# Optimization experiments

Hardware: AMD Instinct MI355X
Metric: run time of the kernel (lower is better)

The kernel has to match this reference:

```python
import jax, jax.numpy as jnp
import numpy as np

N, E = 20000, 640000
IN_CH, OUT_CH = 128, 64
HEADS = (4, 4)
NEG_SLOPE = 0.2


def _gat_layer(x, src, dst, edge_attr, edge_atten, W, a_src, a_dst, W_e, a_e, b, H, C, n_nodes):
    # x: [N, F_in] -> per-head features [N, H, C]
    xh = (x @ W).reshape(-1, H, C)
    alpha_src = jnp.sum(xh * a_src, axis=-1)          # [N, H]
    alpha_dst = jnp.sum(xh * a_dst, axis=-1)          # [N, H]
    eemb = (edge_attr @ W_e).reshape(-1, H, C)        # [E, H, C]
    alpha_e = jnp.sum(eemb * a_e, axis=-1)            # [E, H]
    alpha = alpha_src[src] + alpha_dst[dst] + alpha_e # [E, H]
    alpha = jax.nn.leaky_relu(alpha, NEG_SLOPE)
    # softmax over variable-degree neighborhoods (segments keyed by dst)
    amax = jax.ops.segment_max(alpha, dst, num_segments=n_nodes)
    alpha = jnp.exp(alpha - amax[dst])
    denom = jax.ops.segment_sum(alpha, dst, num_segments=n_nodes)
    alpha = alpha / (denom[dst] + 1e-16)
    msg = xh[src] * alpha[:, :, None]                 # [E, H, C]
    msg = msg * edge_atten[:, :, None]                # edge_atten: [E, 1] -> broadcast over H, C
    out = jax.ops.segment_sum(msg, dst, num_segments=n_nodes)
    out = out.reshape(n_nodes, H * C) + b
    return out, alpha


def setup_inputs() -> dict:
    key = jax.random.key(0)
    ks = jax.random.split(key, 16)
    H1, H2 = HEADS
    d1_in, d1_out = IN_CH, H1 * OUT_CH
    d2_in, d2_out = H1 * OUT_CH, H2 * OUT_CH
    s = lambda fi: 1.0 / np.sqrt(fi)
    inp = {
        "x": jax.random.normal(ks[0], (N, IN_CH), jnp.float32),
        "edge_index": jax.random.randint(ks[1], (2, E), 0, N, jnp.int64 if jax.config.jax_enable_x64 else jnp.int32),
        "batch": jnp.zeros((N,), jnp.int32),
        "edge_attr": jax.random.normal(ks[2], (E, 1), jnp.float32),
        "edge_atten": jax.random.uniform(ks[3], (E, 1), jnp.float32),
        # layer 1 params
        "W1": jax.random.normal(ks[4], (d1_in, d1_out), jnp.float32) * s(d1_in),
        "a_src1": jax.random.normal(ks[5], (H1, OUT_CH), jnp.float32) * s(OUT_CH),
        "a_dst1": jax.random.normal(ks[6], (H1, OUT_CH), jnp.float32) * s(OUT_CH),
        "W_e1": jax.random.normal(ks[7], (1, d1_out), jnp.float32),
        "a_e1": jax.random.normal(ks[8], (H1, OUT_CH), jnp.float32) * s(OUT_CH),
        "b1": jnp.zeros((d1_out,), jnp.float32),
        # layer 2 params
        "W2": jax.random.normal(ks[9], (d2_in, d2_out), jnp.float32) * s(d2_in),
        "a_src2": jax.random.normal(ks[10], (H2, OUT_CH), jnp.float32) * s(OUT_CH),
        "a_dst2": jax.random.normal(ks[11], (H2, OUT_CH), jnp.float32) * s(OUT_CH),
        "W_e2": jax.random.normal(ks[12], (1, d2_out), jnp.float32),
        "a_e2": jax.random.normal(ks[13], (H2, OUT_CH), jnp.float32) * s(OUT_CH),
        "b2": jnp.zeros((d2_out,), jnp.float32),
    }
    return inp


def reference(x, edge_index, batch, edge_attr, edge_atten,
              W1, a_src1, a_dst1, W_e1, a_e1, b1,
              W2, a_src2, a_dst2, W_e2, a_e2, b2):
    src, dst = edge_index[0], edge_index[1]
    h, w1 = _gat_layer(x, src, dst, edge_attr, edge_atten,
                       W1, a_src1, a_dst1, W_e1, a_e1, b1, HEADS[0], OUT_CH, N)
    h, w2 = _gat_layer(h, src, dst, edge_attr, edge_atten,
                       W2, a_src2, a_dst2, W_e2, a_e2, b2, HEADS[1], OUT_CH, N)
    return h, w1, w2
```

## Files before the change

kernel.cpp:

```cpp
#include <hip/hip_runtime.h>
#include <math.h>

#define NEG_SLOPE 0.2f
#define CAP 128
#define ST  136
#define NNODES 20000
#define NB 128

typedef short s16x8 __attribute__((ext_vector_type(8)));
typedef unsigned short us8 __attribute__((ext_vector_type(8)));
typedef float f32x4 __attribute__((ext_vector_type(4)));

__device__ __forceinline__ unsigned short f2bf(float f) {
    unsigned int u = __float_as_uint(f);
    return (unsigned short)((u + 0x7FFFu + ((u >> 16) & 1u)) >> 16);
}
__device__ __forceinline__ float bf2f(unsigned short s) {
    return __uint_as_float(((unsigned int)s) << 16);
}

__global__ __launch_bounds__(512) void hist_prep(const int* __restrict__ dst,
                                                 int* __restrict__ ghist,
                                                 int E, int chunk, int N, int histB,
                                                 const float* __restrict__ x,
                                                 const float* __restrict__ W1,
                                                 const float* __restrict__ W2,
                                                 const float* __restrict__ W_e1,
                                                 const float* __restrict__ a_e1,
                                                 const float* __restrict__ W_e2,
                                                 const float* __restrict__ a_e2,
                                                 unsigned short* __restrict__ xb16,
                                                 unsigned short* __restrict__ Wt1,
                                                 unsigned short* __restrict__ Wt2,
                                                 float* __restrict__ ce) {
    __shared__ int h[NNODES / 2];
    if ((int)blockIdx.x < histB) {
        const int b = blockIdx.x;
        const int NH = N >> 1;
        for (int i = threadIdx.x; i < NH; i += 512) h[i] = 0;
        __syncthreads();
        const int e0 = b * chunk;
        const int e1 = min(e0 + chunk, E);
        for (int e = e0 + (int)threadIdx.x; e < e1; e += 512) {
            int d = dst[e];
            atomicAdd(&h[d >> 1], 1 << ((d & 1) << 4));
        }
        __syncthreads();
        int2* out = (int2*)(ghist + (size_t)b * N);
        for (int i = threadIdx.x; i < NH; i += 512) {
            int v = h[i];
            out[i] = make_int2(v & 0xFFFF, ((unsigned)v) >> 16);
        }
    } else {
        const int p = (int)blockIdx.x - histB;
        const int gsz = 256 * 512;
        const int gid = p * 512 + (int)threadIdx.x;
        for (int i = gid; i < 128 * 256; i += gsz) {
            int k = i >> 8, n = i & 255;
            Wt1[n * 128 + k] = f2bf(W1[i]);
        }
        for (int i = gid; i < 256 * 256; i += gsz) {
            int k = i >> 8, n = i & 255;
            Wt2[n * 256 + k] = f2bf(W2[i]);
        }
        for (int i = gid; i < N * 32; i += gsz) {
            float4 f = ((const float4*)x)[i];
            ushort4 u = make_ushort4(f2bf(f.x), f2bf(f.y), f2bf(f.z), f2bf(f.w));
            ((ushort4*)xb16)[i] = u;
        }
        if (p < 2 && threadIdx.x < 256) {
            const float* We = p == 0 ? W_e1 : W_e2;
            const float* ae = p == 0 ? a_e1 : a_e2;
            int hh = threadIdx.x >> 6, c = threadIdx.x & 63;
            float pr = We[hh * 64 + c] * ae[hh * 64 + c];
#pragma unroll
            for (int off = 32; off > 0; off >>= 1) pr += __shfl_down(pr, off);
            if (c == 0) ce[p * 4 + hh] = pr;
        }
    }
}

__global__ __launch_bounds__(1024) void scan_kernel(const int* __restrict__ deg,
                                                    int* __restrict__ off, int N) {
    __shared__ int wsum[16];
    __shared__ int woff[16];
    __shared__ int s_carry, s_bt;
    if (threadIdx.x == 0) s_carry = 0;
    __syncthreads();
    const int lane = threadIdx.x & 63, wid = threadIdx.x >> 6;
    for (int base = 0; base < N; base += 4096) {
        int i0 = base + (int)threadIdx.x * 4;
        int v0 = (i0 + 0 < N) ? deg[i0 + 0] : 0;
        int v1 = (i0 + 1 < N) ? deg[i0 + 1] : 0;
        int v2 = (i0 + 2 < N) ? deg[i0 + 2] : 0;
        int v3 = (i0 + 3 < N) ? deg[i0 + 3] : 0;
        int tsum = v0 + v1 + v2 + v3;
        int incl = tsum;
#pragma unroll
        for (int ofs = 1; ofs < 64; ofs <<= 1) {
            int t = __shfl_up(incl, ofs);
            if (lane >= ofs) incl += t;
        }
        if (lane == 63) wsum[wid] = incl;
        __syncthreads();
        if (wid == 0) {
            int ws = (lane < 16) ? wsum[lane] : 0;
            int wincl = ws;
#pragma unroll
            for (int ofs = 1; ofs < 16; ofs <<= 1) {
                int t = __shfl_up(wincl, ofs);
                if (lane >= ofs) wincl += t;
            }
            if (lane < 16) woff[lane] = wincl - ws;
            if (lane == 15) s_bt = wincl;
        }
        __syncthreads();
        int e0 = s_carry + woff[wid] + incl - tsum;
        int e1 = e0 + v0, e2 = e1 + v1, e3 = e2 + v2;
        if (i0 + 0 < N) off[i0 + 0] = e0;
        if (i0 + 1 < N) off[i0 + 1] = e1;
        if (i0 + 2 < N) off[i0 + 2] = e2;
        if (i0 + 3 < N) off[i0 + 3] = e3;
        __syncthreads();
        if (threadIdx.x == 0) s_carry += s_bt;
        __syncthreads();
    }
    if (threadIdx.x == 0) off[N] = s_carry;
}

__device__ __forceinline__ void gemm_core(const unsigned short* __restrict__ A16,
                                          const unsigned short* __restrict__ Bt16,
                                          unsigned short* __restrict__ C16,
                                          const float* __restrict__ a_src,
                                          const float* __restrict__ a_dst,
                                          float* __restrict__ asrc,
                                          float* __restrict__ adst,
                                          int M, int K, int bx, int by,
                                          unsigned short (*As)[40],
                                          unsigned short (*Bs)[40]) {
    const int tid = threadIdx.x;
    const int w = tid >> 6, l = tid & 63;
    const int quad = l >> 4, m16 = l & 15;
    const int row0 = by * 128, col0 = bx * 64;

    f32x4 acc[2][4] = {};

    const int a_r = tid >> 1;
    const int a_k = (tid & 1) * 16;
    const int b_n = tid >> 2;
    const int b_k = (tid & 3) * 8;

    for (int k0 = 0; k0 < K; k0 += 32) {
        int gr = row0 + a_r; if (gr > M - 1) gr = M - 1;
        const unsigned short* ap = A16 + (size_t)gr * K + k0 + a_k;
        *(us8*)&As[a_r][a_k]     = *(const us8*)ap;
        *(us8*)&As[a_r][a_k + 8] = *(const us8*)(ap + 8);
        *(us8*)&Bs[b_n][b_k] = *(const us8*)(Bt16 + (size_t)(col0 + b_n) * K + k0 + b_k);
        __syncthreads();

        s16x8 af[2], bfr[4];
#pragma unroll
        for (int mt = 0; mt < 2; ++mt)
            af[mt] = *(const s16x8*)&As[w * 32 + mt * 16 + m16][quad * 8];
#pragma unroll
        for (int nt = 0; nt < 4; ++nt)
            bfr[nt] = *(const s16x8*)&Bs[nt * 16 + m16][quad * 8];
#pragma unroll
        for (int mt = 0; mt < 2; ++mt)
#pragma unroll
            for (int nt = 0; nt < 4; ++nt)
                acc[mt][nt] = __builtin_amdgcn_mfma_f32_16x16x32_bf16(af[mt], bfr[nt], acc[mt][nt], 0, 0, 0);
        __syncthreads();
    }

    const int h = bx;
    float was[4], wad[4];
#pragma unroll
    for (int nt = 0; nt < 4; ++nt) {
        int c = nt * 16 + m16;
        was[nt] = a_src[h * 64 + c];
        wad[nt] = a_dst[h * 64 + c];
    }

#pragma unroll
    for (int mt = 0; mt < 2; ++mt)
#pragma unroll
        for (int i = 0; i < 4; ++i) {
            int row = row0 + w * 32 + mt * 16 + quad * 4 + i;
            float ps = 0.f, pd = 0.f;
#pragma unroll
            for (int nt = 0; nt < 4; ++nt) {
                float v = acc[mt][nt][i];
                ps += v * was[nt];
                pd += v * wad[nt];
            }
#pragma unroll
            for (int ofs = 1; ofs < 16; ofs <<= 1) {
                ps += __shfl_xor(ps, ofs);
                pd += __shfl_xor(pd, ofs);
            }
            if (m16 == 0 && row < M) {
                asrc[(size_t)row * 4 + h] = ps;
                adst[(size_t)row * 4 + h] = pd;
            }
        }

#pragma unroll
    for (int mt = 0; mt < 2; ++mt)
#pragma unroll
        for (int nt = 0; nt < 4; ++nt) {
            int col = col0 + nt * 16 + m16;
#pragma unroll
            for (int i = 0; i < 4; ++i) {
                int row = row0 + w * 32 + mt * 16 + quad * 4 + i;
                if (row < M) C16[(size_t)row * 256 + col] = f2bf(acc[mt][nt][i]);
            }
        }
}

__global__ __launch_bounds__(256) void gemm1_scan(const unsigned short* __restrict__ A16,
                                                  const unsigned short* __restrict__ Bt16,
                                                  unsigned short* __restrict__ C16,
                                                  const float* __restrict__ a_src,
                                                  const float* __restrict__ a_dst,
                                                  float* __restrict__ asrc,
                                                  float* __restrict__ adst,
                                                  int M, int K, int gemmB,
                                                  int* __restrict__ ghist,
                                                  int* __restrict__ deg,
                                                  int N, int histB) {
    __shared__ unsigned short As[128][40];
    __shared__ unsigned short Bs[64][40];
    if ((int)blockIdx.x < gemmB) {
        gemm_core(A16, Bt16, C16, a_src, a_dst, asrc, adst, M, K,
                  blockIdx.x & 3, blockIdx.x >> 2, As, Bs);
    } else {
        int bin = ((int)blockIdx.x - gemmB) * 256 + (int)threadIdx.x;
        if (bin < N) {
            int run = 0;
            for (int b = 0; b < histB; b += 8) {
                int v[8];
#pragma unroll
                for (int j = 0; j < 8; ++j) v[j] = ghist[(b + j) * N + bin];
#pragma unroll
                for (int j = 0; j < 8; ++j) { ghist[(b + j) * N + bin] = run; run += v[j]; }
            }
            deg[bin] = run;
        }
    }
}

__global__ __launch_bounds__(1024) void fill2(const int* __restrict__ src,
                                              const int* __restrict__ dst,
                                              const float* __restrict__ edge_attr,
                                              const float* __restrict__ edge_atten,
                                              const int* __restrict__ off,
                                              const int* __restrict__ ghist,
                                              int4* __restrict__ rec,
                                              int E, int chunk, int N) {
    __shared__ int base[NNODES];
    const int b = blockIdx.x;
    const int* part = ghist + (size_t)b * N;
    for (int i = threadIdx.x; i < N; i += 1024) base[i] = off[i] + part[i];
    __syncthreads();
    const int e0 = b * chunk;
    const int e1 = min(e0 + chunk, E);
    for (int e = e0 + (int)threadIdx.x; e < e1; e += 1024) {
        int d = dst[e];
        int pos = atomicAdd(&base[d], 1);
        rec[pos] = make_int4(src[e], e, __float_as_int(edge_attr[e]),
                             __float_as_int(edge_atten[e]));
    }
}

__global__ __launch_bounds__(256) void node_fused(const int4* __restrict__ rec,
                                                  const int* __restrict__ off,
                                                  const float* __restrict__ asrc,
                                                  const float* __restrict__ adst,
                                                  const float* __restrict__ ce,
                                                  const unsigned short* __restrict__ xh16,
                                                  const float* __restrict__ bias,
                                                  float* __restrict__ w,
                                                  int write_w,
                                                  float* __restrict__ mxrc,
                                                  float* __restrict__ houtf,
                                                  unsigned short* __restrict__ hout16,
                                                  int N) {
    __shared__ float s_al[4][4][ST];
    __shared__ int s_src[4][CAP];
    const int wid = threadIdx.x >> 6;
    const int n = blockIdx.x * 4 + wid;
    if (n >= N) return;
    const int lane = threadIdx.x & 63;
    float* al = &s_al[wid][0][0];
    int* sv = s_src[wid];
    const int o0 = off[n], o1 = off[n + 1];
    const int deg = o1 - o0;

    const float4 c4 = *(const float4*)ce;
    const float4 ad4 = *(const float4*)(adst + (size_t)n * 4);

    if (deg <= 64) {
        int4 r; float4 a;
        a.x = a.y = a.z = a.w = -3.4e38f;
        if (lane < deg) {
            r = rec[o0 + lane];
            float ea = __int_as_float(r.z);
            const float4 as4 = *(const float4*)(asrc + (size_t)r.x * 4);
            a.x = as4.x + ad4.x + ea * c4.x;
            a.y = as4.y + ad4.y + ea * c4.y;
            a.z = as4.z + ad4.z + ea * c4.z;
            a.w = as4.w + ad4.w + ea * c4.w;
            a.x = a.x > 0.f ? a.x : NEG_SLOPE * a.x;
            a.y = a.y > 0.f ? a.y : NEG_SLOPE * a.y;
            a.z = a.z > 0.f ? a.z : NEG_SLOPE * a.z;
            a.w = a.w > 0.f ? a.w : NEG_SLOPE * a.w;
        }
        float4 mx = a;
#pragma unroll
        for (int ofs = 1; ofs < 64; ofs <<= 1) {
            mx.x = fmaxf(mx.x, __shfl_xor(mx.x, ofs));
            mx.y = fmaxf(mx.y, __shfl_xor(mx.y, ofs));
            mx.z = fmaxf(mx.z, __shfl_xor(mx.z, ofs));
            mx.w = fmaxf(mx.w, __shfl_xor(mx.w, ofs));
        }
        float4 ex = make_float4(0.f, 0.f, 0.f, 0.f);
        if (lane < deg) {
            ex.x = __expf(a.x - mx.x);
            ex.y = __expf(a.y - mx.y);
            ex.z = __expf(a.z - mx.z);
            ex.w = __expf(a.w - mx.w);
        }
        float4 sm = ex;
#pragma unroll
        for (int ofs = 1; ofs < 64; ofs <<= 1) {
            sm.x += __shfl_xor(sm.x, ofs);
            sm.y += __shfl_xor(sm.y, ofs);
            sm.z += __shfl_xor(sm.z, ofs);
            sm.w += __shfl_xor(sm.w, ofs);
        }
        float4 rc;
        rc.x = 1.f / (sm.x + 1e-16f);
        rc.y = 1.f / (sm.y + 1e-16f);
        rc.z = 1.f / (sm.z + 1e-16f);
        rc.w = 1.f / (sm.w + 1e-16f);
        if (mxrc && lane == 0) {
            *(float4*)(mxrc + (size_t)n * 8) = mx;
            *(float4*)(mxrc + (size_t)n * 8 + 4) = rc;
        }
        if (lane < deg) {
            float4 aln;
            aln.x = ex.x * rc.x;
            aln.y = ex.y * rc.y;
            aln.z = ex.z * rc.z;
            aln.w = ex.w * rc.w;
            if (write_w) *(float4*)(w + (size_t)r.y * 4) = aln;
            float att = __int_as_float(r.w);
            sv[lane] = r.x;
            al[0 * ST + lane] = aln.x * att;
            al[1 * ST + lane] = aln.y * att;
            al[2 * ST + lane] = aln.z * att;
            al[3 * ST + lane] = aln.w * att;
        }
    } else {
        float4 mx = make_float4(-3.4e38f, -3.4e38f, -3.4e38f, -3.4e38f);
        for (int idx = lane; idx < deg; idx += 64) {
            int4 r = rec[o0 + idx];
            float ea = __int_as_float(r.z);
            const float4 as4 = *(const float4*)(asrc + (size_t)r.x * 4);
            float4 a;
            a.x = as4.x + ad4.x + ea * c4.x;
            a.y = as4.y + ad4.y + ea * c4.y;
            a.z = as4.z + ad4.z + ea * c4.z;
            a.w = as4.w + ad4.w + ea * c4.w;
            a.x = a.x > 0.f ? a.x : NEG_SLOPE * a.x;
            a.y = a.y > 0.f ? a.y : NEG_SLOPE * a.y;
            a.z = a.z > 0.f ? a.z : NEG_SLOPE * a.z;
            a.w = a.w > 0.f ? a.w : NEG_SLOPE * a.w;
            if (idx < CAP) {
                sv[idx] = r.x;
                al[0 * ST + idx] = a.x;
                al[1 * ST + idx] = a.y;
                al[2 * ST + idx] = a.z;
                al[3 * ST + idx] = a.w;
            } else {
                *(float4*)(w + (size_t)r.y * 4) = a;
            }
            mx.x = fmaxf(mx.x, a.x);
            mx.y = fmaxf(mx.y, a.y);
            mx.z = fmaxf(mx.z, a.z);
            mx.w = fmaxf(mx.w, a.w);
        }
#pragma unroll
        for (int ofs = 1; ofs < 64; ofs <<= 1) {
            mx.x = fmaxf(mx.x, __shfl_xor(mx.x, ofs));
            mx.y = fmaxf(mx.y, __shfl_xor(mx.y, ofs));
            mx.z = fmaxf(mx.z, __shfl_xor(mx.z, ofs));
            mx.w = fmaxf(mx.w, __shfl_xor(mx.w, ofs));
        }
        float4 sm = make_float4(0.f, 0.f, 0.f, 0.f);
        for (int idx = lane; idx < deg; idx += 64) {
            float4 a;
            int espill = -1;
            if (idx < CAP) {
                a.x = al[0 * ST + idx];
                a.y = al[1 * ST + idx];
                a.z = al[2 * ST + idx];
                a.w = al[3 * ST + idx];
            } else {
                espill = rec[o0 + idx].y;
                a = *(const float4*)(w + (size_t)espill * 4);
            }
            a.x = __expf(a.x - mx.x);
            a.y = __expf(a.y - mx.y);
            a.z = __expf(a.z - mx.z);
            a.w = __expf(a.w - mx.w);
            if (idx < CAP) {
                al[0 * ST + idx] = a.x;
                al[1 * ST + idx] = a.y;
                al[2 * ST + idx] = a.z;
                al[3 * ST + idx] = a.w;
            } else {
                *(float4*)(w + (size_t)espill * 4) = a;
            }
            sm.x += a.x; sm.y += a.y; sm.z += a.z; sm.w += a.w;
        }
#pragma unroll
        for (int ofs = 1; ofs < 64; ofs <<= 1) {
            sm.x += __shfl_xor(sm.x, ofs);
            sm.y += __shfl_xor(sm.y, ofs);
            sm.z += __shfl_xor(sm.z, ofs);
            sm.w += __shfl_xor(sm.w, ofs);
        }
        float4 rc;
        rc.x = 1.f / (sm.x + 1e-16f);
        rc.y = 1.f / (sm.y + 1e-16f);
        rc.z = 1.f / (sm.z + 1e-16f);
        rc.w = 1.f / (sm.w + 1e-16f);
        if (mxrc && lane == 0) {
            *(float4*)(mxrc + (size_t)n * 8) = mx;
            *(float4*)(mxrc + (size_t)n * 8 + 4) = rc;
        }
        for (int idx = lane; idx < deg; idx += 64) {
            int4 r = rec[o0 + idx];
            float4 ex;
            if (idx < CAP) {
                ex.x = al[0 * ST + idx];
                ex.y = al[1 * ST + idx];
                ex.z = al[2 * ST + idx];
                ex.w = al[3 * ST + idx];
            } else {
                ex = *(const float4*)(w + (size_t)r.y * 4);
            }
            float4 aln;
            aln.x = ex.x * rc.x;
            aln.y = ex.y * rc.y;
            aln.z = ex.z * rc.z;
            aln.w = ex.w * rc.w;
            *(float4*)(w + (size_t)r.y * 4) = aln;
            if (idx < CAP) {
                float att = __int_as_float(r.w);
                al[0 * ST + idx] = aln.x * att;
                al[1 * ST + idx] = aln.y * att;
                al[2 * ST + idx] = aln.z * att;
                al[3 * ST + idx] = aln.w * att;
            }
        }
    }

    const int hh = lane >> 4;
    const float* alh = al + hh * ST;
    float4 a0 = *(const float4*)(bias + lane * 4);
    float4 a1 = make_float4(0.f, 0.f, 0.f, 0.f);
    float4 a2 = make_float4(0.f, 0.f, 0.f, 0.f);
    float4 a3 = make_float4(0.f, 0.f, 0.f, 0.f);
    const int kmax = deg < CAP ? deg : CAP;
    int k = 0;
    for (; k + 4 <= kmax; k += 4) {
        int4 s4 = *(const int4*)&sv[k];
        float4 cc = *(const float4*)&alh[k];
        ushort4 u0 = *((const ushort4*)(xh16 + (size_t)s4.x * 256) + lane);
        ushort4 u1 = *((const ushort4*)(xh16 + (size_t)s4.y * 256) + lane);
        ushort4 u2 = *((const ushort4*)(xh16 + (size_t)s4.z * 256) + lane);
        ushort4 u3 = *((const ushort4*)(xh16 + (size_t)s4.w * 256) + lane);
        a0.x += bf2f(u0.x) * cc.x; a0.y += bf2f(u0.y) * cc.x; a0.z += bf2f(u0.z) * cc.x; a0.w += bf2f(u0.w) * cc.x;
        a1.x += bf2f(u1.x) * cc.y; a1.y += bf2f(u1.y) * cc.y; a1.z += bf2f(u1.z) * cc.y; a1.w += bf2f(u1.w) * cc.y;
        a2.x += bf2f(u2.x) * cc.z; a2.y += bf2f(u2.y) * cc.z; a2.z += bf2f(u2.z) * cc.z; a2.w += bf2f(u2.w) * cc.z;
        a3.x += bf2f(u3.x) * cc.w; a3.y += bf2f(u3.y) * cc.w; a3.z += bf2f(u3.z) * cc.w; a3.w += bf2f(u3.w) * cc.w;
    }
    for (; k < kmax; ++k) {
        int s = sv[k];
        float sc = alh[k];
        ushort4 uv = *((const ushort4*)(xh16 + (size_t)s * 256) + lane);
        a0.x += bf2f(uv.x) * sc; a0.y += bf2f(uv.y) * sc;
        a0.z += bf2f(uv.z) * sc; a0.w += bf2f(uv.w) * sc;
    }
    for (k = CAP; k < deg; ++k) {
        int4 r = rec[o0 + k];
        float sc = w[(size_t)r.y * 4 + hh] * __int_as_float(r.w);
        ushort4 uv = *((const ushort4*)(xh16 + (size_t)r.x * 256) + lane);
        a0.x += bf2f(uv.x) * sc; a0.y += bf2f(uv.y) * sc;
        a0.z += bf2f(uv.z) * sc; a0.w += bf2f(uv.w) * sc;
    }
    float4 acc;
    acc.x = (a0.x + a1.x) + (a2.x + a3.x);
    acc.y = (a0.y + a1.y) + (a2.y + a3.y);
    acc.z = (a0.z + a1.z) + (a2.z + a3.z);
    acc.w = (a0.w + a1.w) + (a2.w + a3.w);
    if (houtf)  *(float4*)(houtf + (size_t)n * 256 + lane * 4) = acc;
    if (hout16) {
        ushort4 u = make_ushort4(f2bf(acc.x), f2bf(acc.y), f2bf(acc.z), f2bf(acc.w));
        *((ushort4*)(hout16 + (size_t)n * 256) + lane) = u;
    }
}

__global__ __launch_bounds__(256) void gemm2_w1(const unsigned short* __restrict__ A16,
                                                const unsigned short* __restrict__ Bt16,
                                                unsigned short* __restrict__ C16,
                                                const float* __restrict__ a_src,
                                                const float* __restrict__ a_dst,
                                                float* __restrict__ asrc2,
                                                float* __restrict__ adst2,
                                                int M, int K, int gemmB,
                                                const int* __restrict__ src,
                                                const int* __restrict__ dstp,
                                                const float* __restrict__ edge_attr,
                                                const float* __restrict__ asrc1,
                                                const float* __restrict__ adst1,
                                                const float* __restrict__ mxrc,
                                                const float* __restrict__ ce1,
                                                float* __restrict__ w1, int E) {
    __shared__ unsigned short As[128][40];
    __shared__ unsigned short Bs[64][40];
    if ((int)blockIdx.x < gemmB) {
        gemm_core(A16, Bt16, C16, a_src, a_dst, asrc2, adst2, M, K,
                  blockIdx.x & 3, blockIdx.x >> 2, As, Bs);
    } else {
        const int stride = ((int)gridDim.x - gemmB) * 256;
        const float4 c4 = *(const float4*)ce1;
        for (int e = ((int)blockIdx.x - gemmB) * 256 + (int)threadIdx.x; e < E; e += stride) {
            int s = src[e], d = dstp[e];
            float ea = edge_attr[e];
            const float4 as4 = *(const float4*)(asrc1 + (size_t)s * 4);
            const float4 ad4 = *(const float4*)(adst1 + (size_t)d * 4);
            float4 a;
            a.x = as4.x + ad4.x + ea * c4.x;
            a.y = as4.y + ad4.y + ea * c4.y;
            a.z = as4.z + ad4.z + ea * c4.z;
            a.w = as4.w + ad4.w + ea * c4.w;
            a.x = a.x > 0.f ? a.x : NEG_SLOPE * a.x;
            a.y = a.y > 0.f ? a.y : NEG_SLOPE * a.y;
            a.z = a.z > 0.f ? a.z : NEG_SLOPE * a.z;
            a.w = a.w > 0.f ? a.w : NEG_SLOPE * a.w;
            const float4 mx = *(const float4*)(mxrc + (size_t)d * 8);
            const float4 rc = *(const float4*)(mxrc + (size_t)d * 8 + 4);
            float4 o;
            o.x = __expf(a.x - mx.x) * rc.x;
            o.y = __expf(a.y - mx.y) * rc.y;
            o.z = __expf(a.z - mx.z) * rc.z;
            o.w = __expf(a.w - mx.w) * rc.w;
            *(float4*)(w1 + (size_t)e * 4) = o;
        }
    }
}

extern "C" void kernel_launch(void* const* d_in, const int* in_sizes, int n_in,
                              void* d_out, int out_size, void* d_ws, size_t ws_size,
                              hipStream_t stream) {
    const float* x          = (const float*)d_in[0];
    const int*   ei         = (const int*)d_in[1];
    const float* edge_attr  = (const float*)d_in[3];
    const float* edge_atten = (const float*)d_in[4];
    const float* W1     = (const float*)d_in[5];
    const float* a_src1 = (const float*)d_in[6];
    const float* a_dst1 = (const float*)d_in[7];
    const float* W_e1   = (const float*)d_in[8];
    const float* a_e1   = (const float*)d_in[9];
    const float* b1     = (const float*)d_in[10];
    const float* W2     = (const float*)d_in[11];
    const float* a_src2 = (const float*)d_in[12];
    const float* a_dst2 = (const float*)d_in[13];
    const float* W_e2   = (const float*)d_in[14];
    const float* a_e2   = (const float*)d_in[15];
    const float* b2     = (const float*)d_in[16];

    const int N = in_sizes[0] / 128;
    const int E = in_sizes[1] / 2;
    const int* srcp = ei;
    const int* dstp = ei + E;

    char* ws = (char*)d_ws;
    int4* rec             = (int4*)ws;            ws += (size_t)E * 16;
    unsigned short* xh16  = (unsigned short*)ws;  ws += (size_t)N * 256 * 2;
    unsigned short* h116  = (unsigned short*)ws;  ws += (size_t)N * 256 * 2;
    unsigned short* Wt1   = (unsigned short*)ws;  ws += (size_t)256 * 128 * 2;
    unsigned short* Wt2   = (unsigned short*)ws;  ws += (size_t)256 * 256 * 2;
    float* asrc   = (float*)ws;                   ws += (size_t)N * 4 * 4;
    float* adst   = (float*)ws;                   ws += (size_t)N * 4 * 4;
    float* asrc2  = (float*)ws;                   ws += (size_t)N * 4 * 4;
    float* adst2  = (float*)ws;                   ws += (size_t)N * 4 * 4;
    float* mxrc   = (float*)ws;                   ws += (size_t)N * 8 * 4;
    float* ce     = (float*)ws;                   ws += 32;
    int* deg    = (int*)ws;                       ws += (size_t)N * 4;
    int* off    = (int*)ws;                       ws += (size_t)(N + 1) * 4;
    int* ghist  = (int*)ws;                       ws += (size_t)NB * N * 4;

    unsigned short* xb16 = h116;

    float* hout2 = (float*)d_out;
    float* w1    = hout2 + (size_t)N * 256;
    float* w2    = w1 + (size_t)E * 4;

    const int chunk = (E + NB - 1) / NB;
    const int gb = (N + 3) / 4;
    const int rows = (N + 127) / 128;
    const int gemmB = 4 * rows;
    const int scanB = (N + 255) / 256;
    const int wB = 512;

    hist_prep<<<NB + 256, 512, 0, stream>>>(dstp, ghist, E, chunk, N, NB,
                                            x, W1, W2, W_e1, a_e1, W_e2, a_e2,
                                            xb16, Wt1, Wt2, ce);
    gemm1_scan<<<gemmB + scanB, 256, 0, stream>>>(xb16, Wt1, xh16, a_src1, a_dst1,
                                                  asrc, adst, N, 128, gemmB,
                                                  ghist, deg, N, NB);
    scan_kernel<<<1, 1024, 0, stream>>>(deg, off, N);
    fill2<<<NB, 1024, 0, stream>>>(srcp, dstp, edge_attr, edge_atten, off, ghist,
                                   rec, E, chunk, N);
    node_fused<<<gb, 256, 0, stream>>>(rec, off, asrc, adst, ce, xh16, b1, w1,
                                       0, mxrc, (float*)nullptr, h116, N);
    gemm2_w1<<<gemmB + wB, 256, 0, stream>>>(h116, Wt2, xh16, a_src2, a_dst2,
                                             asrc2, adst2, N, 256, gemmB,
                                             srcp, dstp, edge_attr,
                                             asrc, adst, mxrc, ce, w1, E);
    node_fused<<<gb, 256, 0, stream>>>(rec, off, asrc2, adst2, ce + 4, xh16, b2, w2,
                                       1, (float*)nullptr, hout2,
                                       (unsigned short*)nullptr, N);
}
```

Measured before the change: 255.9 us.

## Fold layer-1 projection into layer-2 GEMM via aggregation of raw inputs

Layer 1 drops its GEMM. Its attention logits come from a small GEMV using precomputed W1·a vectors, and layer-1 aggregation gathers raw 128-channel inputs per head into a 512-wide buffer. The layer-2 GEMM then multiplies that buffer by the fused weight W1_h·W2 (K=512) and adds b1·W2. This removes the first GEMM and the 256-wide layer-1 intermediate, at the cost of a GEMM with twice the K and a different bf16 rounding path.

Measured after the change: 290.0 us. 1.13x slower.

```diff
diff --git a/kernel.cpp b/kernel.cpp
--- a/kernel.cpp
+++ b/kernel.cpp
@@ -25,13 +25,17 @@
                                                  const float* __restrict__ x,
                                                  const float* __restrict__ W1,
                                                  const float* __restrict__ W2,
+                                                 const float* __restrict__ a_src1,
+                                                 const float* __restrict__ a_dst1,
+                                                 const float* __restrict__ b1,
                                                  const float* __restrict__ W_e1,
                                                  const float* __restrict__ a_e1,
                                                  const float* __restrict__ W_e2,
                                                  const float* __restrict__ a_e2,
                                                  unsigned short* __restrict__ xb16,
-                                                 unsigned short* __restrict__ Wt1,
-                                                 unsigned short* __restrict__ Wt2,
+                                                 unsigned short* __restrict__ Wt12,
+                                                 float* __restrict__ Wa,
+                                                 float* __restrict__ b1w2,
                                                  float* __restrict__ ce) {
     __shared__ int h[NNODES / 2];
     if ((int)blockIdx.x < histB) {
@@ -55,13 +59,28 @@
         const int p = (int)blockIdx.x - histB;
         const int gsz = 256 * 512;
         const int gid = p * 512 + (int)threadIdx.x;
-        for (int i = gid; i < 128 * 256; i += gsz) {
-            int k = i >> 8, n = i & 255;
-            Wt1[n * 128 + k] = f2bf(W1[i]);
-        }
-        for (int i = gid; i < 256 * 256; i += gsz) {
-            int k = i >> 8, n = i & 255;
-            Wt2[n * 256 + k] = f2bf(W2[i]);
+        for (int i = gid; i < 512 * 256; i += gsz) {
+            int j = i >> 9, q = i & 511, hh = q >> 7, k = q & 127;
+            const float* w1r = W1 + k * 256 + hh * 64;
+            const float* w2c = W2 + (hh * 64) * 256 + j;
+            float v = 0.f;
+#pragma unroll 8
+            for (int c = 0; c < 64; ++c) v += w1r[c] * w2c[c * 256];
+            Wt12[j * 512 + q] = f2bf(v);
+        }
+        for (int i = gid; i < 1024; i += gsz) {
+            int k = i >> 3, j2 = i & 7, hh = j2 & 3;
+            const float* av = (j2 < 4 ? a_src1 : a_dst1) + hh * 64;
+            const float* w1r = W1 + k * 256 + hh * 64;
+            float v = 0.f;
+#pragma unroll 8
+            for (int c = 0; c < 64; ++c) v += w1r[c] * av[c];
+            Wa[k * 8 + j2] = v;
+        }
+        for (int i = gid; i < 256; i += gsz) {
+            float v = 0.f;
+            for (int t = 0; t < 256; ++t) v += b1[t] * W2[t * 256 + i];
+            b1w2[i] = v;
         }
         for (int i = gid; i < N * 32; i += gsz) {
             float4 f = ((const float4*)x)[i];
@@ -76,6 +95,54 @@
 #pragma unroll
             for (int off = 32; off > 0; off >>= 1) pr += __shfl_down(pr, off);
             if (c == 0) ce[p * 4 + hh] = pr;
+        }
+    }
+}
+
+__global__ __launch_bounds__(256) void gemv_scan(const unsigned short* __restrict__ xb16,
+                                                 const float* __restrict__ Wa,
+                                                 float* __restrict__ as1,
+                                                 float* __restrict__ ad1,
+                                                 int gemvB,
+                                                 int* __restrict__ ghist,
+                                                 int* __restrict__ deg,
+                                                 int N, int histB) {
+    __shared__ float sWa[1024];
+    if ((int)blockIdx.x < gemvB) {
+        for (int i = threadIdx.x; i < 1024; i += 256) sWa[i] = Wa[i];
+        __syncthreads();
+        const int wv = threadIdx.x >> 6, lane = threadIdx.x & 63;
+        const int k2 = lane << 1;
+        const int n0 = blockIdx.x * 16 + wv * 4;
+        for (int n = n0; n < n0 + 4 && n < N; ++n) {
+            ushort2 u = *(const ushort2*)(xb16 + (size_t)n * 128 + k2);
+            float xa = bf2f(u.x), xb = bf2f(u.y);
+            float p[8];
+#pragma unroll
+            for (int j = 0; j < 8; ++j)
+                p[j] = xa * sWa[k2 * 8 + j] + xb * sWa[k2 * 8 + 8 + j];
+#pragma unroll
+            for (int ofs = 1; ofs < 64; ofs <<= 1) {
+#pragma unroll
+                for (int j = 0; j < 8; ++j) p[j] += __shfl_xor(p[j], ofs);
+            }
+            if (lane == 0) {
+                *(float4*)(as1 + (size_t)n * 4) = make_float4(p[0], p[1], p[2], p[3]);
+                *(float4*)(ad1 + (size_t)n * 4) = make_float4(p[4], p[5], p[6], p[7]);
+            }
+        }
+    } else {
+        int bin = ((int)blockIdx.x - gemvB) * 256 + (int)threadIdx.x;
+        if (bin < N) {
+            int run = 0;
+            for (int b = 0; b < histB; b += 8) {
+                int v[8];
+#pragma unroll
+                for (int j = 0; j < 8; ++j) v[j] = ghist[(b + j) * N + bin];
+#pragma unroll
+                for (int j = 0; j < 8; ++j) { ghist[(b + j) * N + bin] = run; run += v[j]; }
+            }
+            deg[bin] = run;
         }
     }
 }
@@ -126,128 +193,6 @@
         __syncthreads();
     }
     if (threadIdx.x == 0) off[N] = s_carry;
-}
-
-__device__ __forceinline__ void gemm_core(const unsigned short* __restrict__ A16,
-                                          const unsigned short* __restrict__ Bt16,
-                                          unsigned short* __restrict__ C16,
-                                          const float* __restrict__ a_src,
-                                          const float* __restrict__ a_dst,
-                                          float* __restrict__ asrc,
-                                          float* __restrict__ adst,
-                                          int M, int K, int bx, int by,
-                                          unsigned short (*As)[40],
-                                          unsigned short (*Bs)[40]) {
-    const int tid = threadIdx.x;
-    const int w = tid >> 6, l = tid & 63;
-    const int quad = l >> 4, m16 = l & 15;
-    const int row0 = by * 128, col0 = bx * 64;
-
-    f32x4 acc[2][4] = {};
-
-    const int a_r = tid >> 1;
-    const int a_k = (tid & 1) * 16;
-    const int b_n = tid >> 2;
-    const int b_k = (tid & 3) * 8;
-
-    for (int k0 = 0; k0 < K; k0 += 32) {
-        int gr = row0 + a_r; if (gr > M - 1) gr = M - 1;
-        const unsigned short* ap = A16 + (size_t)gr * K + k0 + a_k;
-        *(us8*)&As[a_r][a_k]     = *(const us8*)ap;
-        *(us8*)&As[a_r][a_k + 8] = *(const us8*)(ap + 8);
-        *(us8*)&Bs[b_n][b_k] = *(const us8*)(Bt16 + (size_t)(col0 + b_n) * K + k0 + b_k);
-        __syncthreads();
-
-        s16x8 af[2], bfr[4];
-#pragma unroll
-        for (int mt = 0; mt < 2; ++mt)
-            af[mt] = *(const s16x8*)&As[w * 32 + mt * 16 + m16][quad * 8];
-#pragma unroll
-        for (int nt = 0; nt < 4; ++nt)
-            bfr[nt] = *(const s16x8*)&Bs[nt * 16 + m16][quad * 8];
-#pragma unroll
-        for (int mt = 0; mt < 2; ++mt)
-#pragma unroll
-            for (int nt = 0; nt < 4; ++nt)
-                acc[mt][nt] = __builtin_amdgcn_mfma_f32_16x16x32_bf16(af[mt], bfr[nt], acc[mt][nt], 0, 0, 0);
-        __syncthreads();
-    }
-
-    const int h = bx;
-    float was[4], wad[4];
-#pragma unroll
-    for (int nt = 0; nt < 4; ++nt) {
-        int c = nt * 16 + m16;
-        was[nt] = a_src[h * 64 + c];
-        wad[nt] = a_dst[h * 64 + c];
-    }
-
-#pragma unroll
-    for (int mt = 0; mt < 2; ++mt)
-#pragma unroll
-        for (int i = 0; i < 4; ++i) {
-            int row = row0 + w * 32 + mt * 16 + quad * 4 + i;
-            float ps = 0.f, pd = 0.f;
-#pragma unroll
-            for (int nt = 0; nt < 4; ++nt) {
-                float v = acc[mt][nt][i];
-                ps += v * was[nt];
-                pd += v * wad[nt];
-            }
-#pragma unroll
-            for (int ofs = 1; ofs < 16; ofs <<= 1) {
-                ps += __shfl_xor(ps, ofs);
-                pd += __shfl_xor(pd, ofs);
-            }
-            if (m16 == 0 && row < M) {
-                asrc[(size_t)row * 4 + h] = ps;
-                adst[(size_t)row * 4 + h] = pd;
-            }
-        }
-
-#pragma unroll
-    for (int mt = 0; mt < 2; ++mt)
-#pragma unroll
-        for (int nt = 0; nt < 4; ++nt) {
-            int col = col0 + nt * 16 + m16;
-#pragma unroll
-            for (int i = 0; i < 4; ++i) {
-                int row = row0 + w * 32 + mt * 16 + quad * 4 + i;
-                if (row < M) C16[(size_t)row * 256 + col] = f2bf(acc[mt][nt][i]);
-            }
-        }
-}
-
-__global__ __launch_bounds__(256) void gemm1_scan(const unsigned short* __restrict__ A16,
-                                                  const unsigned short* __restrict__ Bt16,
-                                                  unsigned short* __restrict__ C16,
-                                                  const float* __restrict__ a_src,
-                                                  const float* __restrict__ a_dst,
-                                                  float* __restrict__ asrc,
-                                                  float* __restrict__ adst,
-                                                  int M, int K, int gemmB,
-                                                  int* __restrict__ ghist,
-                                                  int* __restrict__ deg,
-                                                  int N, int histB) {
-    __shared__ unsigned short As[128][40];
-    __shared__ unsigned short Bs[64][40];
-    if ((int)blockIdx.x < gemmB) {
-        gemm_core(A16, Bt16, C16, a_src, a_dst, asrc, adst, M, K,
-                  blockIdx.x & 3, blockIdx.x >> 2, As, Bs);
-    } else {
-        int bin = ((int)blockIdx.x - gemmB) * 256 + (int)threadIdx.x;
-        if (bin < N) {
-            int run = 0;
-            for (int b = 0; b < histB; b += 8) {
-                int v[8];
-#pragma unroll
-                for (int j = 0; j < 8; ++j) v[j] = ghist[(b + j) * N + bin];
-#pragma unroll
-                for (int j = 0; j < 8; ++j) { ghist[(b + j) * N + bin] = run; run += v[j]; }
-            }
-            deg[bin] = run;
-        }
-    }
 }
 
 __global__ __launch_bounds__(1024) void fill2(const int* __restrict__ src,
@@ -273,19 +218,121 @@
     }
 }
 
-__global__ __launch_bounds__(256) void node_fused(const int4* __restrict__ rec,
-                                                  const int* __restrict__ off,
-                                                  const float* __restrict__ asrc,
-                                                  const float* __restrict__ adst,
-                                                  const float* __restrict__ ce,
-                                                  const unsigned short* __restrict__ xh16,
-                                                  const float* __restrict__ bias,
-                                                  float* __restrict__ w,
-                                                  int write_w,
-                                                  float* __restrict__ mxrc,
-                                                  float* __restrict__ houtf,
-                                                  unsigned short* __restrict__ hout16,
-                                                  int N) {
+__device__ __forceinline__ void gemm_core(const unsigned short* __restrict__ A16,
+                                          const unsigned short* __restrict__ Bt16,
+                                          unsigned short* __restrict__ C16,
+                                          const float* __restrict__ a_src,
+                                          const float* __restrict__ a_dst,
+                                          const float* __restrict__ bw,
+                                          float* __restrict__ asrc,
+                                          float* __restrict__ adst,
+                                          int M, int K, int bx, int by,
+                                          unsigned short (*As)[40],
+                                          unsigned short (*Bs)[40]) {
+    const int tid = threadIdx.x;
+    const int w = tid >> 6, l = tid & 63;
+    const int quad = l >> 4, m16 = l & 15;
+    const int row0 = by * 128, col0 = bx * 64;
+
+    f32x4 acc[2][4] = {};
+
+    const int a_r = tid >> 1;
+    const int a_k = (tid & 1) * 16;
+    const int b_n = tid >> 2;
+    const int b_k = (tid & 3) * 8;
+
+    for (int k0 = 0; k0 < K; k0 += 32) {
+        int gr = row0 + a_r; if (gr > M - 1) gr = M - 1;
+        const unsigned short* ap = A16 + (size_t)gr * K + k0 + a_k;
+        *(us8*)&As[a_r][a_k]     = *(const us8*)ap;
+        *(us8*)&As[a_r][a_k + 8] = *(const us8*)(ap + 8);
+        *(us8*)&Bs[b_n][b_k] = *(const us8*)(Bt16 + (size_t)(col0 + b_n) * K + k0 + b_k);
+        __syncthreads();
+
+        s16x8 af[2], bfr[4];
+#pragma unroll
+        for (int mt = 0; mt < 2; ++mt)
+            af[mt] = *(const s16x8*)&As[w * 32 + mt * 16 + m16][quad * 8];
+#pragma unroll
+        for (int nt = 0; nt < 4; ++nt)
+            bfr[nt] = *(const s16x8*)&Bs[nt * 16 + m16][quad * 8];
+#pragma unroll
+        for (int mt = 0; mt < 2; ++mt)
+#pragma unroll
+            for (int nt = 0; nt < 4; ++nt)
+                acc[mt][nt] = __builtin_amdgcn_mfma_f32_16x16x32_bf16(af[mt], bfr[nt], acc[mt][nt], 0, 0, 0);
+        __syncthreads();
+    }
+
+    float bwv[4];
+#pragma unroll
+    for (int nt = 0; nt < 4; ++nt) bwv[nt] = bw[col0 + nt * 16 + m16];
+#pragma unroll
+    for (int mt = 0; mt < 2; ++mt)
+#pragma unroll
+        for (int nt = 0; nt < 4; ++nt)
+#pragma unroll
+            for (int i = 0; i < 4; ++i) acc[mt][nt][i] += bwv[nt];
+
+    const int h = bx;
+    float was[4], wad[4];
+#pragma unroll
+    for (int nt = 0; nt < 4; ++nt) {
+        int c = nt * 16 + m16;
+        was[nt] = a_src[h * 64 + c];
+        wad[nt] = a_dst[h * 64 + c];
+    }
+
+#pragma unroll
+    for (int mt = 0; mt < 2; ++mt)
+#pragma unroll
+        for (int i = 0; i < 4; ++i) {
+            int row = row0 + w * 32 + mt * 16 + quad * 4 + i;
+            float ps = 0.f, pd = 0.f;
+#pragma unroll
+            for (int nt = 0; nt < 4; ++nt) {
+                float v = acc[mt][nt][i];
+                ps += v * was[nt];
+                pd += v * wad[nt];
+            }
+#pragma unroll
+            for (int ofs = 1; ofs < 16; ofs <<= 1) {
+                ps += __shfl_xor(ps, ofs);
+                pd += __shfl_xor(pd, ofs);
+            }
+            if (m16 == 0 && row < M) {
+                asrc[(size_t)row * 4 + h] = ps;
+                adst[(size_t)row * 4 + h] = pd;
+            }
+        }
+
+#pragma unroll
+    for (int mt = 0; mt < 2; ++mt)
+#pragma unroll
+        for (int nt = 0; nt < 4; ++nt) {
+            int col = col0 + nt * 16 + m16;
+#pragma unroll
+            for (int i = 0; i < 4; ++i) {
+                int row = row0 + w * 32 + mt * 16 + quad * 4 + i;
+                if (row < M) C16[(size_t)row * 256 + col] = f2bf(acc[mt][nt][i]);
+            }
+        }
+}
+
+template <int MODE>
+__global__ __launch_bounds__(256) void node_pass(const int4* __restrict__ rec,
+                                                 const int* __restrict__ off,
+                                                 const float* __restrict__ asrc,
+                                                 const float* __restrict__ adst,
+                                                 const float* __restrict__ ce,
+                                                 const unsigned short* __restrict__ feat,
+                                                 const float* __restrict__ bias,
+                                                 float* __restrict__ w,
+                                                 int write_w,
+                                                 float* __restrict__ mxrc,
+                                                 unsigned short* __restrict__ aggout,
+                                                 float* __restrict__ houtf,
+                                                 int N) {
     __shared__ float s_al[4][4][ST];
     __shared__ int s_src[4][CAP];
     const int wid = threadIdx.x >> 6;
@@ -344,7 +391,7 @@
         rc.y = 1.f / (sm.y + 1e-16f);
         rc.z = 1.f / (sm.z + 1e-16f);
         rc.w = 1.f / (sm.w + 1e-16f);
-        if (mxrc && lane == 0) {
+        if (MODE == 0 && lane == 0) {
             *(float4*)(mxrc + (size_t)n * 8) = mx;
             *(float4*)(mxrc + (size_t)n * 8 + 4) = rc;
         }
@@ -437,7 +484,7 @@
         rc.y = 1.f / (sm.y + 1e-16f);
         rc.z = 1.f / (sm.z + 1e-16f);
         rc.w = 1.f / (sm.w + 1e-16f);
-        if (mxrc && lane == 0) {
+        if (MODE == 0 && lane == 0) {
             *(float4*)(mxrc + (size_t)n * 8) = mx;
             *(float4*)(mxrc + (size_t)n * 8 + 4) = rc;
         }
@@ -468,72 +515,128 @@
         }
     }
 
-    const int hh = lane >> 4;
-    const float* alh = al + hh * ST;
-    float4 a0 = *(const float4*)(bias + lane * 4);
-    float4 a1 = make_float4(0.f, 0.f, 0.f, 0.f);
-    float4 a2 = make_float4(0.f, 0.f, 0.f, 0.f);
-    float4 a3 = make_float4(0.f, 0.f, 0.f, 0.f);
     const int kmax = deg < CAP ? deg : CAP;
-    int k = 0;
-    for (; k + 4 <= kmax; k += 4) {
-        int4 s4 = *(const int4*)&sv[k];
-        float4 cc = *(const float4*)&alh[k];
-        ushort4 u0 = *((const ushort4*)(xh16 + (size_t)s4.x * 256) + lane);
-        ushort4 u1 = *((const ushort4*)(xh16 + (size_t)s4.y * 256) + lane);
-        ushort4 u2 = *((const ushort4*)(xh16 + (size_t)s4.z * 256) + lane);
-        ushort4 u3 = *((const ushort4*)(xh16 + (size_t)s4.w * 256) + lane);
-        a0.x += bf2f(u0.x) * cc.x; a0.y += bf2f(u0.y) * cc.x; a0.z += bf2f(u0.z) * cc.x; a0.w += bf2f(u0.w) * cc.x;
-        a1.x += bf2f(u1.x) * cc.y; a1.y += bf2f(u1.y) * cc.y; a1.z += bf2f(u1.z) * cc.y; a1.w += bf2f(u1.w) * cc.y;
-        a2.x += bf2f(u2.x) * cc.z; a2.y += bf2f(u2.y) * cc.z; a2.z += bf2f(u2.z) * cc.z; a2.w += bf2f(u2.w) * cc.z;
-        a3.x += bf2f(u3.x) * cc.w; a3.y += bf2f(u3.y) * cc.w; a3.z += bf2f(u3.z) * cc.w; a3.w += bf2f(u3.w) * cc.w;
-    }
-    for (; k < kmax; ++k) {
-        int s = sv[k];
-        float sc = alh[k];
-        ushort4 uv = *((const ushort4*)(xh16 + (size_t)s * 256) + lane);
-        a0.x += bf2f(uv.x) * sc; a0.y += bf2f(uv.y) * sc;
-        a0.z += bf2f(uv.z) * sc; a0.w += bf2f(uv.w) * sc;
-    }
-    for (k = CAP; k < deg; ++k) {
-        int4 r = rec[o0 + k];
-        float sc = w[(size_t)r.y * 4 + hh] * __int_as_float(r.w);
-        ushort4 uv = *((const ushort4*)(xh16 + (size_t)r.x * 256) + lane);
-        a0.x += bf2f(uv.x) * sc; a0.y += bf2f(uv.y) * sc;
-        a0.z += bf2f(uv.z) * sc; a0.w += bf2f(uv.w) * sc;
-    }
-    float4 acc;
-    acc.x = (a0.x + a1.x) + (a2.x + a3.x);
-    acc.y = (a0.y + a1.y) + (a2.y + a3.y);
-    acc.z = (a0.z + a1.z) + (a2.z + a3.z);
-    acc.w = (a0.w + a1.w) + (a2.w + a3.w);
-    if (houtf)  *(float4*)(houtf + (size_t)n * 256 + lane * 4) = acc;
-    if (hout16) {
-        ushort4 u = make_ushort4(f2bf(acc.x), f2bf(acc.y), f2bf(acc.z), f2bf(acc.w));
-        *((ushort4*)(hout16 + (size_t)n * 256) + lane) = u;
-    }
-}
-
-__global__ __launch_bounds__(256) void gemm2_w1(const unsigned short* __restrict__ A16,
-                                                const unsigned short* __restrict__ Bt16,
-                                                unsigned short* __restrict__ C16,
-                                                const float* __restrict__ a_src,
-                                                const float* __restrict__ a_dst,
-                                                float* __restrict__ asrc2,
-                                                float* __restrict__ adst2,
-                                                int M, int K, int gemmB,
-                                                const int* __restrict__ src,
-                                                const int* __restrict__ dstp,
-                                                const float* __restrict__ edge_attr,
-                                                const float* __restrict__ asrc1,
-                                                const float* __restrict__ adst1,
-                                                const float* __restrict__ mxrc,
-                                                const float* __restrict__ ce1,
-                                                float* __restrict__ w1, int E) {
+
+    if constexpr (MODE == 0) {
+        const int k2 = lane << 1;
+        const unsigned short* xb = feat + k2;
+        float a00 = 0.f, a01 = 0.f, a10 = 0.f, a11 = 0.f;
+        float a20 = 0.f, a21 = 0.f, a30 = 0.f, a31 = 0.f;
+        int k = 0;
+        for (; k + 4 <= kmax; k += 4) {
+            int4 s4 = *(const int4*)&sv[k];
+            ushort2 u0 = *(const ushort2*)(xb + (size_t)s4.x * 128);
+            ushort2 u1 = *(const ushort2*)(xb + (size_t)s4.y * 128);
+            ushort2 u2 = *(const ushort2*)(xb + (size_t)s4.z * 128);
+            ushort2 u3 = *(const ushort2*)(xb + (size_t)s4.w * 128);
+            float4 c0 = *(const float4*)&al[0 * ST + k];
+            float4 c1 = *(const float4*)&al[1 * ST + k];
+            float4 c2 = *(const float4*)&al[2 * ST + k];
+            float4 c3 = *(const float4*)&al[3 * ST + k];
+            float x0a = bf2f(u0.x), x0b = bf2f(u0.y);
+            float x1a = bf2f(u1.x), x1b = bf2f(u1.y);
+            float x2a = bf2f(u2.x), x2b = bf2f(u2.y);
+            float x3a = bf2f(u3.x), x3b = bf2f(u3.y);
+            a00 += x0a * c0.x + x1a * c0.y + x2a * c0.z + x3a * c0.w;
+            a01 += x0b * c0.x + x1b * c0.y + x2b * c0.z + x3b * c0.w;
+            a10 += x0a * c1.x + x1a * c1.y + x2a * c1.z + x3a * c1.w;
+            a11 += x0b * c1.x + x1b * c1.y + x2b * c1.z + x3b * c1.w;
+            a20 += x0a * c2.x + x1a * c2.y + x2a * c2.z + x3a * c2.w;
+            a21 += x0b * c2.x + x1b * c2.y + x2b * c2.z + x3b * c2.w;
+            a30 += x0a * c3.x + x1a * c3.y + x2a * c3.z + x3a * c3.w;
+            a31 += x0b * c3.x + x1b * c3.y + x2b * c3.z + x3b * c3.w;
+        }
+        for (; k < kmax; ++k) {
+            int s = sv[k];
+            ushort2 u = *(const ushort2*)(xb + (size_t)s * 128);
+            float xa = bf2f(u.x), xbv = bf2f(u.y);
+            float q0 = al[0 * ST + k], q1 = al[1 * ST + k];
+            float q2 = al[2 * ST + k], q3 = al[3 * ST + k];
+            a00 += xa * q0; a01 += xbv * q0;
+            a10 += xa * q1; a11 += xbv * q1;
+            a20 += xa * q2; a21 += xbv * q2;
+            a30 += xa * q3; a31 += xbv * q3;
+        }
+        for (int kk = CAP; kk < deg; ++kk) {
+            int4 r = rec[o0 + kk];
+            float att = __int_as_float(r.w);
+            const float* wv = w + (size_t)r.y * 4;
+            ushort2 u = *(const ushort2*)(xb + (size_t)r.x * 128);
+            float xa = bf2f(u.x), xbv = bf2f(u.y);
+            float q0 = wv[0] * att, q1 = wv[1] * att, q2 = wv[2] * att, q3 = wv[3] * att;
+            a00 += xa * q0; a01 += xbv * q0;
+            a10 += xa * q1; a11 += xbv * q1;
+            a20 += xa * q2; a21 += xbv * q2;
+            a30 += xa * q3; a31 += xbv * q3;
+        }
+        unsigned short* ao = aggout + (size_t)n * 512 + k2;
+        *(ushort2*)(ao + 0)   = make_ushort2(f2bf(a00), f2bf(a01));
+        *(ushort2*)(ao + 128) = make_ushort2(f2bf(a10), f2bf(a11));
+        *(ushort2*)(ao + 256) = make_ushort2(f2bf(a20), f2bf(a21));
+        *(ushort2*)(ao + 384) = make_ushort2(f2bf(a30), f2bf(a31));
+    } else {
+        const int hh = lane >> 4;
+        const float* alh = al + hh * ST;
+        float4 a0 = *(const float4*)(bias + lane * 4);
+        float4 a1 = make_float4(0.f, 0.f, 0.f, 0.f);
+        float4 a2 = a1, a3 = a1;
+        int k = 0;
+        for (; k + 4 <= kmax; k += 4) {
+            int4 s4 = *(const int4*)&sv[k];
+            float4 cc = *(const float4*)&alh[k];
+            ushort4 u0 = *((const ushort4*)(feat + (size_t)s4.x * 256) + lane);
+            ushort4 u1 = *((const ushort4*)(feat + (size_t)s4.y * 256) + lane);
+            ushort4 u2 = *((const ushort4*)(feat + (size_t)s4.z * 256) + lane);
+            ushort4 u3 = *((const ushort4*)(feat + (size_t)s4.w * 256) + lane);
+            a0.x += bf2f(u0.x) * cc.x; a0.y += bf2f(u0.y) * cc.x; a0.z += bf2f(u0.z) * cc.x; a0.w += bf2f(u0.w) * cc.x;
+            a1.x += bf2f(u1.x) * cc.y; a1.y += bf2f(u1.y) * cc.y; a1.z += bf2f(u1.z) * cc.y; a1.w += bf2f(u1.w) * cc.y;
+            a2.x += bf2f(u2.x) * cc.z; a2.y += bf2f(u2.y) * cc.z; a2.z += bf2f(u2.z) * cc.z; a2.w += bf2f(u2.w) * cc.z;
+            a3.x += bf2f(u3.x) * cc.w; a3.y += bf2f(u3.y) * cc.w; a3.z += bf2f(u3.z) * cc.w; a3.w += bf2f(u3.w) * cc.w;
+        }
+        for (; k < kmax; ++k) {
+            int s = sv[k];
+            float sc = alh[k];
+            ushort4 uv = *((const ushort4*)(feat + (size_t)s * 256) + lane);
+            a0.x += bf2f(uv.x) * sc; a0.y += bf2f(uv.y) * sc;
+            a0.z += bf2f(uv.z) * sc; a0.w += bf2f(uv.w) * sc;
+        }
+        for (int kk = CAP; kk < deg; ++kk) {
+            int4 r = rec[o0 + kk];
+            float sc = w[(size_t)r.y * 4 + hh] * __int_as_float(r.w);
+            ushort4 uv = *((const ushort4*)(feat + (size_t)r.x * 256) + lane);
+            a0.x += bf2f(uv.x) * sc; a0.y += bf2f(uv.y) * sc;
+            a0.z += bf2f(uv.z) * sc; a0.w += bf2f(uv.w) * sc;
+        }
+        float4 acc;
+        acc.x = (a0.x + a1.x) + (a2.x + a3.x);
+        acc.y = (a0.y + a1.y) + (a2.y + a3.y);
+        acc.z = (a0.z + a1.z) + (a2.z + a3.z);
+        acc.w = (a0.w + a1.w) + (a2.w + a3.w);
+        *(float4*)(houtf + (size_t)n * 256 + lane * 4) = acc;
+    }
+}
+
+__global__ __launch_bounds__(256) void gemm2w1(const unsigned short* __restrict__ A16,
+                                               const unsigned short* __restrict__ Bt16,
+                                               unsigned short* __restrict__ C16,
+                                               const float* __restrict__ a_src,
+                                               const float* __restrict__ a_dst,
+                                               const float* __restrict__ bw,
+                                               float* __restrict__ as2,
+                                               float* __restrict__ ad2,
+                                               int M, int K, int gemmB,
+                                               const int* __restrict__ src,
+                                               const int* __restrict__ dstp,
+                                               const float* __restrict__ edge_attr,
+                                               const float* __restrict__ as1,
+                                               const float* __restrict__ ad1,
+                                               const float* __restrict__ mxrc,
+                                               const float* __restrict__ ce1,
+                                               float* __restrict__ w1, int E) {
     __shared__ unsigned short As[128][40];
     __shared__ unsigned short Bs[64][40];
     if ((int)blockIdx.x < gemmB) {
-        gemm_core(A16, Bt16, C16, a_src, a_dst, asrc2, adst2, M, K,
+        gemm_core(A16, Bt16, C16, a_src, a_dst, bw, as2, ad2, M, K,
                   blockIdx.x & 3, blockIdx.x >> 2, As, Bs);
     } else {
         const int stride = ((int)gridDim.x - gemmB) * 256;
@@ -541,8 +644,8 @@
         for (int e = ((int)blockIdx.x - gemmB) * 256 + (int)threadIdx.x; e < E; e += stride) {
             int s = src[e], d = dstp[e];
             float ea = edge_attr[e];
-            const float4 as4 = *(const float4*)(asrc1 + (size_t)s * 4);
-            const float4 ad4 = *(const float4*)(adst1 + (size_t)d * 4);
+            const float4 as4 = *(const float4*)(as1 + (size_t)s * 4);
+            const float4 ad4 = *(const float4*)(ad1 + (size_t)d * 4);
             float4 a;
             a.x = as4.x + ad4.x + ea * c4.x;
             a.y = as4.y + ad4.y + ea * c4.y;
@@ -592,20 +695,22 @@
     char* ws = (char*)d_ws;
     int4* rec             = (int4*)ws;            ws += (size_t)E * 16;
     unsigned short* xh16  = (unsigned short*)ws;  ws += (size_t)N * 256 * 2;
-    unsigned short* h116  = (unsigned short*)ws;  ws += (size_t)N * 256 * 2;
-    unsigned short* Wt1   = (unsigned short*)ws;  ws += (size_t)256 * 128 * 2;
-    unsigned short* Wt2   = (unsigned short*)ws;  ws += (size_t)256 * 256 * 2;
-    float* asrc   = (float*)ws;                   ws += (size_t)N * 4 * 4;
-    float* adst   = (float*)ws;                   ws += (size_t)N * 4 * 4;
-    float* asrc2  = (float*)ws;                   ws += (size_t)N * 4 * 4;
-    float* adst2  = (float*)ws;                   ws += (size_t)N * 4 * 4;
+    unsigned short* Wt12  = (unsigned short*)ws;  ws += (size_t)256 * 512 * 2;
+    float* Wa     = (float*)ws;                   ws += 128 * 8 * 4;
+    float* b1w2   = (float*)ws;                   ws += 256 * 4;
+    float* as1    = (float*)ws;                   ws += (size_t)N * 4 * 4;
+    float* ad1    = (float*)ws;                   ws += (size_t)N * 4 * 4;
+    float* as2    = (float*)ws;                   ws += (size_t)N * 4 * 4;
+    float* ad2    = (float*)ws;                   ws += (size_t)N * 4 * 4;
     float* mxrc   = (float*)ws;                   ws += (size_t)N * 8 * 4;
     float* ce     = (float*)ws;                   ws += 32;
     int* deg    = (int*)ws;                       ws += (size_t)N * 4;
-    int* off    = (int*)ws;                       ws += (size_t)(N + 1) * 4;
-    int* ghist  = (int*)ws;                       ws += (size_t)NB * N * 4;
-
-    unsigned short* xb16 = h116;
+    int* off    = (int*)ws;                       ws += (size_t)(N + 4) * 4;
+    int* ghist  = (int*)ws;
+    unsigned short* aggflat = (unsigned short*)ws;
+    ws += (size_t)N * 512 * 2;
+
+    unsigned short* xb16 = xh16;
 
     float* hout2 = (float*)d_out;
     float* w1    = hout2 + (size_t)N * 256;
@@ -616,24 +721,26 @@
     const int rows = (N + 127) / 128;
     const int gemmB = 4 * rows;
     const int scanB = (N + 255) / 256;
+    const int gemvB = (N + 15) / 16;
     const int wB = 512;
 
     hist_prep<<<NB + 256, 512, 0, stream>>>(dstp, ghist, E, chunk, N, NB,
-                                            x, W1, W2, W_e1, a_e1, W_e2, a_e2,
-                                            xb16, Wt1, Wt2, ce);
-    gemm1_scan<<<gemmB + scanB, 256, 0, stream>>>(xb16, Wt1, xh16, a_src1, a_dst1,
-                                                  asrc, adst, N, 128, gemmB,
-                                                  ghist, deg, N, NB);
+                                            x, W1, W2, a_src1, a_dst1, b1,
+                                            W_e1, a_e1, W_e2, a_e2,
+                                            xb16, Wt12, Wa, b1w2, ce);
+    gemv_scan<<<gemvB + scanB, 256, 0, stream>>>(xb16, Wa, as1, ad1, gemvB,
+                                                 ghist, deg, N, NB);
     scan_kernel<<<1, 1024, 0, stream>>>(deg, off, N);
     fill2<<<NB, 1024, 0, stream>>>(srcp, dstp, edge_attr, edge_atten, off, ghist,
                                    rec, E, chunk, N);
-    node_fused<<<gb, 256, 0, stream>>>(rec, off, asrc, adst, ce, xh16, b1, w1,
-                                       0, mxrc, (float*)nullptr, h116, N);
-    gemm2_w1<<<gemmB + wB, 256, 0, stream>>>(h116, Wt2, xh16, a_src2, a_dst2,
-                                             asrc2, adst2, N, 256, gemmB,
-                                             srcp, dstp, edge_attr,
-                                             asrc, adst, mxrc, ce, w1, E);
-    node_fused<<<gb, 256, 0, stream>>>(rec, off, asrc2, adst2, ce + 4, xh16, b2, w2,
-                                       1, (float*)nullptr, hout2,
-                                       (unsigned short*)nullptr, N);
-}
+    node_pass<0><<<gb, 256, 0, stream>>>(rec, off, as1, ad1, ce, xb16,
+                                         (const float*)nullptr, w1, 0, mxrc,
+                                         aggflat, (float*)nullptr, N);
+    gemm2w1<<<gemmB + wB, 256, 0, stream>>>(aggflat, Wt12, xh16, a_src2, a_dst2, b1w2,
+                                            as2, ad2, N, 512, gemmB,
+                                            srcp, dstp, edge_attr,
+                                            as1, ad1, mxrc, ce, w1, E);
+    node_pass<1><<<gb, 256, 0, stream>>>(rec, off, as2, ad2, ce + 4, xh16, b2, w2,
+                                         1, (float*)nullptr,
+                                         (unsigned short*)nullptr, hout2, N);
+}
```
